# Optimization experiments

Hardware: AMD Instinct MI355X
Metric: run time of the kernel (lower is better)

Reference implementation:

```python
import jax, jax.numpy as jnp
import numpy as np
from jax.ops import segment_sum, segment_max

N = 100000   # nodes
E = 300000   # directed edges (3-regular fullerene cages)
F_IN = 16    # num_node_features
D = 128      # hidden_dim
H = 8        # heads
C = D // H   # per-head channels = 16
L = 4        # num_layers
G = 1600     # number of graphs in the batch
EPS = 1e-5   # BatchNorm eps
NEG_SLOPE = 0.2  # GATConv leaky_relu slope


def setup_inputs() -> dict:
    key = jax.random.key(0)
    ks = jax.random.split(key, 16)
    x = jax.random.normal(ks[0], (N, F_IN), jnp.float32)
    edge_index = jax.random.randint(ks[1], (2, E), 0, N, dtype=jnp.int64)
    batch = jnp.sort(jax.random.randint(ks[2], (N,), 0, G, dtype=jnp.int64))
    def w(k, shape, fan_in):
        return jax.random.normal(k, shape, jnp.float32) / np.sqrt(fan_in)
    return {
        "x": x, "edge_index": edge_index, "batch": batch,
        "Wp": w(ks[3], (F_IN, D), F_IN), "bp": jnp.zeros((D,), jnp.float32),
        "Wg": w(ks[4], (L, D, D), D),                       # per-layer GAT lin weight
        "asrc": w(ks[5], (L, H, C), C), "adst": w(ks[6], (L, H, C), C),
        "bg": jnp.zeros((L, D), jnp.float32),               # GAT bias
        "gamma": jnp.ones((L, D), jnp.float32), "beta": jnp.zeros((L, D), jnp.float32),
        "hW1": w(ks[7], (3, D, D // 2), D), "hb1": jnp.zeros((3, D // 2), jnp.float32),
        "hW2": w(ks[8], (3, D // 2, 1), D // 2), "hb2": jnp.zeros((3, 1), jnp.float32),
    }


def _gat_layer(x, W, att_src, att_dst, bias, src, dst):
    # PyG GATConv: linear transform per head, additive attention, scatter-softmax over dst
    xh = (x @ W).reshape(N, H, C)                      # [N,H,C]
    a_src = (xh * att_src).sum(-1)                     # [N,H]
    a_dst = (xh * att_dst).sum(-1)                     # [N,H]
    e = jax.nn.leaky_relu(a_src[src] + a_dst[dst], NEG_SLOPE)   # [E',H]
    m = segment_max(e, dst, num_segments=N)            # stable softmax per destination
    ex = jnp.exp(e - m[dst])
    denom = segment_sum(ex, dst, num_segments=N)       # > 0 (self-loops present)
    alpha = ex / denom[dst]                            # [E',H]
    out = segment_sum(alpha[:, :, None] * xh[src], dst, num_segments=N)  # [N,H,C]
    return out.reshape(N, D) + bias


def _forward(x, Wp, bp, Wg, asrc, adst, bg, gamma, beta, hW1, hb1, hW2, hb2,
             edge_index, batch):
    # add self loops (GATConv default add_self_loops=True)
    loop = jnp.arange(N, dtype=edge_index.dtype)
    src = jnp.concatenate([edge_index[0], loop])
    dst = jnp.concatenate([edge_index[1], loop])
    h = jax.nn.relu(x @ Wp + bp)
    for i in range(L):
        h = _gat_layer(h, Wg[i], asrc[i], adst[i], bg[i], src, dst)
        mu = h.mean(0)
        var = ((h - mu) ** 2).mean(0)                   # biased var (BN training math)
        h = (h - mu) / jnp.sqrt(var + EPS) * gamma[i] + beta[i]
        h = jax.nn.relu(h)                              # dropout off (eval)
    # global mean pool over graphs
    counts = segment_sum(jnp.ones((N,), h.dtype), batch, num_segments=G)
    pooled = segment_sum(h, batch, num_segments=G) / jnp.maximum(counts, 1.0)[:, None]
    # 3 output heads: Linear -> ReLU -> Linear(1)
    hid = jax.nn.relu(jnp.einsum('gd,kdm->kgm', pooled, hW1) + hb1[:, None, :])
    out = jnp.einsum('kgm,kmo->kgo', hid, hW2) + hb2[:, None, :]   # [3,G,1]
    return out[:, :, 0].T                               # [G,3]


def reference(x, edge_index, batch, Wp, bp, Wg, asrc, adst, bg, gamma, beta,
              hW1, hb1, hW2, hb2):
    return _forward(x, Wp, bp, Wg, asrc, adst, bg, gamma, beta,
                    hW1, hb1, hW2, hb2, edge_index, batch)
```

## Files before the change

### kernel.cpp

```cpp
#include <hip/hip_runtime.h>

#define D 128
#define NH 8
#define CH 16
#define NEG 0.2f
#define BN_EPS 1e-5f
#define MAXDEG 32
#define NSLICE 32
#define WROWS 144

typedef unsigned int uint;
typedef unsigned short ushort;
typedef __attribute__((ext_vector_type(8))) short bfrag;
typedef __attribute__((ext_vector_type(4))) float ffrag;

__device__ __forceinline__ float bf_lo(uint u){ return __uint_as_float(u << 16); }
__device__ __forceinline__ float bf_hi(uint u){ return __uint_as_float(u & 0xffff0000u); }
__device__ __forceinline__ float bf2f(ushort s){ return __uint_as_float(((uint)s) << 16); }
__device__ __forceinline__ ushort f2b(float f){
  uint u = __float_as_uint(f);
  u += 0x7fffu + ((u >> 16) & 1u);
  return (ushort)(u >> 16);
}

__global__ void k_scatter(const int* __restrict__ ei, int* __restrict__ deg,
                          int* __restrict__ col, int E){
  int e = blockIdx.x*blockDim.x + threadIdx.x;
  if (e < E){
    int d = ei[E + e];
    int pos = atomicAdd(&deg[d], 1);
    if (pos < MAXDEG) col[(size_t)d*MAXDEG + pos] = ei[e];
  }
}

__global__ void k_setup(const float* __restrict__ x, const float* __restrict__ Wp,
                        const float* __restrict__ bp, ushort* __restrict__ h,
                        const int* __restrict__ batch, int* __restrict__ gs,
                        const float* __restrict__ Wg, const float* __restrict__ asrc,
                        const float* __restrict__ adst, ushort* __restrict__ WtB,
                        int n, int G, int WTOT, int bInit, int bGb, int bWp){
  int bid = blockIdx.x;
  int t = threadIdx.x;
  if (bid < bInit){
    int i = bid*256 + t;
    if (i >= n*32) return;
    int nid = i >> 5, d4 = (i & 31)*4;
    const float* xr = x + nid*16;
    float s[4] = { bp[d4], bp[d4+1], bp[d4+2], bp[d4+3] };
#pragma unroll
    for (int k = 0; k < 16; k++){
      float xv = xr[k];
      const float* wr = Wp + k*D + d4;
      s[0] += xv*wr[0]; s[1] += xv*wr[1]; s[2] += xv*wr[2]; s[3] += xv*wr[3];
    }
    uint2 o;
    o.x = ((uint)f2b(fmaxf(s[0],0.f))) | (((uint)f2b(fmaxf(s[1],0.f))) << 16);
    o.y = ((uint)f2b(fmaxf(s[2],0.f))) | (((uint)f2b(fmaxf(s[3],0.f))) << 16);
    *(uint2*)(h + (size_t)nid*D + d4) = o;
  } else if (bid < bInit + bGb){
    int i = (bid - bInit)*256 + t;
    if (i >= n) return;
    int b = batch[i];
    int bpv = (i == 0) ? -1 : batch[i-1];
    for (int g = bpv + 1; g <= b; g++) gs[g] = i;
    if (i == n-1) for (int g = b + 1; g <= G; g++) gs[g] = n;
  } else if (bid < bInit + bGb + bWp){
    int i = (bid - bInit - bGb)*256 + t;
    if (i >= WTOT) return;
    int l = i >> 14, r = i & 16383, nn = r >> 7, kk = r & 127;
    WtB[(size_t)l*WROWS*D + nn*D + kk] = f2b(Wg[(size_t)l*16384 + kk*128 + nn]);
  } else {
    int i = (bid - bInit - bGb - bWp)*256 + t;
    int wscTot = (WTOT >> 14)*16*128;
    if (i >= wscTot) return;
    int l = i >> 11, r = i & 2047, j = r >> 7, k = r & 127;
    const float* wrow = Wg + (size_t)l*16384 + k*128;
    float s = 0.f;
    if (j < 8){
      const float* av = asrc + l*128 + j*16;
#pragma unroll
      for (int c = 0; c < 16; c++) s += wrow[j*16 + c] * av[c];
    } else {
      const float* av = adst + l*128 + (j - 8)*16;
#pragma unroll
      for (int c = 0; c < 16; c++) s += wrow[(j - 8)*16 + c] * av[c];
    }
    WtB[(size_t)l*WROWS*D + (128 + j)*D + k] = f2b(s);
  }
}

__global__ __launch_bounds__(512) void k_gemm(const ushort* __restrict__ hin,
                                              const ushort* __restrict__ WtB,
                                              ushort* __restrict__ xh,
                                              float* __restrict__ sc2,
                                              const float* __restrict__ bnsum,
                                              const float* __restrict__ gamma,
                                              const float* __restrict__ beta,
                                              int n, int first){
  __shared__ __align__(16) ushort wL[WROWS*136];
  __shared__ float sS[128], sB[128];
  int t = threadIdx.x;
  int wid = t >> 6, lane = t & 63, l15 = lane & 15, quad = lane >> 4;
  int n0 = blockIdx.x * 256;
  int rbase = wid*32;

  if (t < 128){
    float sc, sh;
    if (first){ sc = 1.f; sh = 0.f; }
    else {
      float s = 0.f, s2 = 0.f;
#pragma unroll 8
      for (int sl = 0; sl < NSLICE; sl++){
        s  += bnsum[sl*256 + t];
        s2 += bnsum[sl*256 + 128 + t];
      }
      float invn = 1.0f / (float)n;
      float mu = s * invn;
      float var = s2 * invn - mu*mu;
      sc = gamma[t] * rsqrtf(var + BN_EPS);
      sh = beta[t] - mu*sc;
    }
    sS[t] = sc; sB[t] = sh;
  }
#pragma unroll
  for (int i = 0; i < 5; i++){
    int u = t + i*512;
    if (u < WROWS*16){
      int r = u >> 4, c8 = u & 15;
      *(uint4*)(wL + r*136 + c8*8) = *(const uint4*)(WtB + (size_t)r*D + c8*8);
    }
  }
  __syncthreads();

  bfrag a[2][4];
#pragma unroll
  for (int mt = 0; mt < 2; mt++){
    int row = n0 + rbase + mt*16 + l15;
#pragma unroll
    for (int ks = 0; ks < 4; ks++){
      union { bfrag b; ushort us[8]; } in, ov;
      in.b = (bfrag){0,0,0,0,0,0,0,0};
      if (row < n) in.b = *(const bfrag*)(hin + (size_t)row*D + ks*32 + quad*8);
      int kb = ks*32 + quad*8;
#pragma unroll
      for (int j = 0; j < 8; j++){
        float f = bf2f(in.us[j])*sS[kb + j] + sB[kb + j];
        ov.us[j] = f2b(f > 0.f ? f : 0.f);
      }
      a[mt][ks] = ov.b;
    }
  }

  ffrag acc[2][9];
#pragma unroll
  for (int mt = 0; mt < 2; mt++)
#pragma unroll
    for (int nt = 0; nt < 9; nt++) acc[mt][nt] = (ffrag){0.f,0.f,0.f,0.f};

#pragma unroll
  for (int nt = 0; nt < 9; nt++){
#pragma unroll
    for (int ks = 0; ks < 4; ks++){
      bfrag b = *(const bfrag*)(wL + (nt*16 + l15)*136 + ks*32 + quad*8);
      acc[0][nt] = __builtin_amdgcn_mfma_f32_16x16x32_bf16(a[0][ks], b, acc[0][nt], 0, 0, 0);
      acc[1][nt] = __builtin_amdgcn_mfma_f32_16x16x32_bf16(a[1][ks], b, acc[1][nt], 0, 0, 0);
    }
  }

#pragma unroll
  for (int mt = 0; mt < 2; mt++)
#pragma unroll
    for (int r = 0; r < 4; r++){
      int grow = n0 + rbase + mt*16 + quad*4 + r;
      if (grow < n){
        sc2[(size_t)grow*16 + l15] = acc[mt][8][r];
        ushort* xr = xh + (size_t)grow*D + l15;
#pragma unroll
        for (int nt = 0; nt < 8; nt++)
          xr[nt*16] = f2b(acc[mt][nt][r]);
      }
    }
}

__global__ __launch_bounds__(1024) void k_agg(const uint* __restrict__ xh32,
                                              const float* __restrict__ sc2,
                                              const int* __restrict__ deg,
                                              const int* __restrict__ col,
                                              const float* __restrict__ bg,
                                              ushort* __restrict__ hout,
                                              float* __restrict__ bnsum, int n){
  int wv = threadIdx.x >> 6;
  int l  = threadIdx.x & 63;
  int hs = l & 7;
  int jc = l >> 3;
  int nid = blockIdx.x*16 + wv;

  float s0=0.f, s1=0.f, q0=0.f, q1=0.f;

  if (nid < n){
    const int* cb = col + nid*MAXDEG;
    int cnt = deg[nid];
    int idx[8];
#pragma unroll
    for (int jj = 0; jj < 8; jj++) idx[jj] = cb[jj];
    float ad = sc2[nid*16 + 8 + hs];
    float as = sc2[nid*16 + hs];
    uint selfv = xh32[nid*64 + l];
    float av = sc2[idx[jc]*16 + hs];
    float xv0[8], xv1[8];
#pragma unroll
    for (int jj = 0; jj < 8; jj++){
      uint v = xh32[idx[jj]*64 + l];
      xv0[jj] = bf_lo(v); xv1[jj] = bf_hi(v);
    }
    if (cnt > MAXDEG) cnt = MAXDEG;
    int cc = cnt < 8 ? cnt : 8;
    float e0 = as + ad; e0 = e0 > 0.f ? e0 : NEG*e0;
    float m = e0, dnm = 1.f;
    float acc0 = bf_lo(selfv), acc1 = bf_hi(selfv);

    float e = -1e30f;
    if (jc < cc){ float ee = av + ad; e = ee > 0.f ? ee : NEG*ee; }
    float mc = e;
    mc = fmaxf(mc, __shfl_xor(mc, 8));
    mc = fmaxf(mc, __shfl_xor(mc, 16));
    mc = fmaxf(mc, __shfl_xor(mc, 32));
    float mn = fmaxf(m, mc);
    float rsc = __expf(m - mn);
    float w = (jc < cc) ? __expf(e - mn) : 0.f;
    float ws = w;
    ws += __shfl_xor(ws, 8);
    ws += __shfl_xor(ws, 16);
    ws += __shfl_xor(ws, 32);
    dnm = dnm*rsc + ws;
    m = mn;
    float rc = __shfl(rsc, jc);
    acc0 *= rc; acc1 *= rc;
#pragma unroll
    for (int jj = 0; jj < 8; jj++){
      float wj = __shfl(w, jj*8 + jc);
      acc0 += wj * xv0[jj];
      acc1 += wj * xv1[jj];
    }
    for (int c0 = 8; c0 < cnt; c0 += 8){
      int cc2 = cnt - c0; if (cc2 > 8) cc2 = 8;
#pragma unroll
      for (int jj = 0; jj < 8; jj++) idx[jj] = cb[c0 + jj];
      float av2 = sc2[idx[jc]*16 + hs];
#pragma unroll
      for (int jj = 0; jj < 8; jj++){
        uint v = xh32[idx[jj]*64 + l];
        xv0[jj] = bf_lo(v); xv1[jj] = bf_hi(v);
      }
      float e2 = -1e30f;
      if (jc < cc2){ float ee = av2 + ad; e2 = ee > 0.f ? ee : NEG*ee; }
      float mc2 = e2;
      mc2 = fmaxf(mc2, __shfl_xor(mc2, 8));
      mc2 = fmaxf(mc2, __shfl_xor(mc2, 16));
      mc2 = fmaxf(mc2, __shfl_xor(mc2, 32));
      float mn2 = fmaxf(m, mc2);
      float rsc2 = __expf(m - mn2);
      float w2 = (jc < cc2) ? __expf(e2 - mn2) : 0.f;
      float ws2 = w2;
      ws2 += __shfl_xor(ws2, 8);
      ws2 += __shfl_xor(ws2, 16);
      ws2 += __shfl_xor(ws2, 32);
      dnm = dnm*rsc2 + ws2;
      m = mn2;
      float rc2 = __shfl(rsc2, jc);
      acc0 *= rc2; acc1 *= rc2;
#pragma unroll
      for (int jj = 0; jj < 8; jj++){
        float wj = __shfl(w2, jj*8 + jc);
        acc0 += wj * xv0[jj];
        acc1 += wj * xv1[jj];
      }
    }
    float df = __shfl(dnm, jc);
    float inv = 1.0f / df;
    float b0 = bg[2*l], b1 = bg[2*l + 1];
    float o0 = acc0*inv + b0, o1 = acc1*inv + b1;
    uint p = ((uint)f2b(o0)) | (((uint)f2b(o1)) << 16);
    ((uint*)hout)[nid*64 + l] = p;
    s0 = o0; s1 = o1; q0 = o0*o0; q1 = o1*o1;
  }

  __shared__ float red[16][64][4];
  red[wv][l][0] = s0; red[wv][l][1] = s1; red[wv][l][2] = q0; red[wv][l][3] = q1;
  __syncthreads();
  if (wv == 0){
    float t0 = 0.f, t1 = 0.f, t2 = 0.f, t3 = 0.f;
#pragma unroll
    for (int k = 0; k < 16; k++){
      t0 += red[k][l][0]; t1 += red[k][l][1];
      t2 += red[k][l][2]; t3 += red[k][l][3];
    }
    float* bs = bnsum + (blockIdx.x & (NSLICE - 1))*256;
    atomicAdd(&bs[2*l],       t0);
    atomicAdd(&bs[2*l + 1],   t1);
    atomicAdd(&bs[128 + 2*l], t2);
    atomicAdd(&bs[129 + 2*l], t3);
  }
}

__global__ __launch_bounds__(128) void k_poolheads(const ushort* __restrict__ h,
                                                   const int* __restrict__ gs,
                                                   const float* __restrict__ bnsum,
                                                   const float* __restrict__ gamma,
                                                   const float* __restrict__ beta,
                                                   const float* __restrict__ hW1,
                                                   const float* __restrict__ hb1,
                                                   const float* __restrict__ hW2,
                                                   const float* __restrict__ hb2,
                                                   float* __restrict__ out, int n){
  int g = blockIdx.x;
  int t = threadIdx.x;
  __shared__ float sp[128];
  int st = gs[g], en = gs[g + 1];
  float sm = 0.f, s2 = 0.f;
#pragma unroll 8
  for (int sl = 0; sl < NSLICE; sl++){
    sm += bnsum[sl*256 + t];
    s2 += bnsum[sl*256 + 128 + t];
  }
  float invn = 1.0f / (float)n;
  float mu = sm * invn;
  float var = s2 * invn - mu*mu;
  float sc = gamma[t] * rsqrtf(var + BN_EPS);
  float sh = beta[t] - mu*sc;
  float s = 0.f;
  for (int r = st; r < en; r++){
    float v = bf2f(h[(size_t)r*D + t]) * sc + sh;
    s += v > 0.f ? v : 0.f;
  }
  float cnt = (float)(en - st);
  sp[t] = s / fmaxf(cnt, 1.0f);
  __syncthreads();
  int wv = t >> 6, m = t & 63;
  for (int k = wv; k < 3; k += 2){
    float acc = hb1[k*64 + m];
    const float* w = hW1 + k*8192 + m;
#pragma unroll 16
    for (int d = 0; d < 128; d++) acc += sp[d] * w[d*64];
    float val = fmaxf(acc, 0.f) * hW2[k*64 + m];
#pragma unroll
    for (int off = 32; off; off >>= 1) val += __shfl_down(val, off);
    if (m == 0) out[(size_t)g*3 + k] = val + hb2[k];
  }
}

extern "C" void kernel_launch(void* const* d_in, const int* in_sizes, int n_in,
                              void* d_out, int out_size, void* d_ws, size_t ws_size,
                              hipStream_t stream){
  const float* x    = (const float*)d_in[0];
  const int*   ei   = (const int*)d_in[1];
  const int*   batch= (const int*)d_in[2];
  const float* Wp   = (const float*)d_in[3];
  const float* bp   = (const float*)d_in[4];
  const float* Wg   = (const float*)d_in[5];
  const float* asrc = (const float*)d_in[6];
  const float* adst = (const float*)d_in[7];
  const float* bg   = (const float*)d_in[8];
  const float* gamma= (const float*)d_in[9];
  const float* beta = (const float*)d_in[10];
  const float* hW1  = (const float*)d_in[11];
  const float* hb1  = (const float*)d_in[12];
  const float* hW2  = (const float*)d_in[13];
  const float* hb2  = (const float*)d_in[14];
  float* out = (float*)d_out;

  const int E = in_sizes[1] / 2;
  const int N = in_sizes[2];
  const int G = out_size / 3;
  const int WTOT = in_sizes[5];
  const int L = WTOT / 16384;

  char* w = (char*)d_ws;
  auto alloc = [&](size_t bytes){ char* p = w; w += (bytes + 255) & ~(size_t)255; return p; };
  ushort* h     = (ushort*)alloc((size_t)N*D*2);
  ushort* xh    = (ushort*)alloc((size_t)N*D*2);
  float* sc2    = (float*)alloc((size_t)N*16*4);
  int*   deg    = (int*)  alloc((size_t)N*4);
  int*   col    = (int*)  alloc(((size_t)N*MAXDEG + 64)*4);
  float* bnsumL = (float*)alloc((size_t)4*NSLICE*256*4);
  char*  zend   = w;
  int*   gs     = (int*)  alloc((size_t)(G + 1)*4);
  ushort* WtB   = (ushort*)alloc((size_t)L*WROWS*D*2);

  hipMemsetAsync(deg, 0, (size_t)(zend - (char*)deg), stream);
  k_scatter<<<(E + 255)/256, 256, 0, stream>>>(ei, deg, col, E);

  const int bInit = (N*32 + 255)/256;
  const int bGb   = (N + 255)/256;
  const int bWp   = (WTOT + 255)/256;
  const int bWsc  = (WTOT/8 + 255)/256;
  k_setup<<<bInit + bGb + bWp + bWsc, 256, 0, stream>>>(
      x, Wp, bp, h, batch, gs, Wg, asrc, adst, WtB,
      N, G, WTOT, bInit, bGb, bWp);

  for (int l = 0; l < 4; l++){
    float* bnPrev = bnsumL + (size_t)(l - 1)*NSLICE*256;
    float* bnCur  = bnsumL + (size_t)l*NSLICE*256;
    k_gemm<<<(N + 255)/256, 512, 0, stream>>>(h, WtB + (size_t)l*WROWS*D, xh, sc2,
                                              l == 0 ? bnCur : bnPrev,
                                              gamma + l*D, beta + l*D, N, l == 0);
    k_agg<<<(N + 15)/16, 1024, 0, stream>>>((const uint*)xh, sc2, deg, col,
                                            bg + l*D, h, bnCur, N);
  }

  k_poolheads<<<G, 128, 0, stream>>>(h, gs, bnsumL + (size_t)3*NSLICE*256,
                                     gamma + 3*D, beta + 3*D,
                                     hW1, hb1, hW2, hb2, out, N);
}
```

Baseline: 394.2 us.

## Process four nodes per wavefront in GAT aggregation to batch gathers

The aggregation kernel now has each wavefront handle four destination nodes instead of one. It loads the column indices with int4 vector loads and issues all first-chunk neighbor gathers for the four nodes together, to raise memory-level parallelism and hide gather latency. Invalid indices are clamped so the col buffer no longer needs zeroing, and it moves out of the memset range. In exchange it uses more registers per thread, launches a quarter as many waves, and creates less contention on the BN partial-sum atomics.

```diff
diff --git a/kernel.cpp b/kernel.cpp
--- a/kernel.cpp
+++ b/kernel.cpp
@@ -8,6 +8,7 @@
 #define MAXDEG 32
 #define NSLICE 32
 #define WROWS 144
+#define NPW 4
 
 typedef unsigned int uint;
 typedef unsigned short ushort;
@@ -182,116 +183,185 @@
     }
 }
 
-__global__ __launch_bounds__(1024) void k_agg(const uint* __restrict__ xh32,
-                                              const float* __restrict__ sc2,
-                                              const int* __restrict__ deg,
-                                              const int* __restrict__ col,
-                                              const float* __restrict__ bg,
-                                              ushort* __restrict__ hout,
-                                              float* __restrict__ bnsum, int n){
+__global__ __launch_bounds__(512) void k_agg(const uint* __restrict__ xh32,
+                                             const float* __restrict__ sc2,
+                                             const int* __restrict__ deg,
+                                             const int* __restrict__ col,
+                                             const float* __restrict__ bg,
+                                             ushort* __restrict__ hout,
+                                             float* __restrict__ bnsum, int n){
   int wv = threadIdx.x >> 6;
   int l  = threadIdx.x & 63;
   int hs = l & 7;
   int jc = l >> 3;
-  int nid = blockIdx.x*16 + wv;
-
-  float s0=0.f, s1=0.f, q0=0.f, q1=0.f;
-
-  if (nid < n){
-    const int* cb = col + nid*MAXDEG;
-    int cnt = deg[nid];
-    int idx[8];
-#pragma unroll
-    for (int jj = 0; jj < 8; jj++) idx[jj] = cb[jj];
-    float ad = sc2[nid*16 + 8 + hs];
-    float as = sc2[nid*16 + hs];
-    uint selfv = xh32[nid*64 + l];
-    float av = sc2[idx[jc]*16 + hs];
-    float xv0[8], xv1[8];
-#pragma unroll
-    for (int jj = 0; jj < 8; jj++){
-      uint v = xh32[idx[jj]*64 + l];
-      xv0[jj] = bf_lo(v); xv1[jj] = bf_hi(v);
-    }
-    if (cnt > MAXDEG) cnt = MAXDEG;
-    int cc = cnt < 8 ? cnt : 8;
-    float e0 = as + ad; e0 = e0 > 0.f ? e0 : NEG*e0;
-    float m = e0, dnm = 1.f;
-    float acc0 = bf_lo(selfv), acc1 = bf_hi(selfv);
-
-    float e = -1e30f;
-    if (jc < cc){ float ee = av + ad; e = ee > 0.f ? ee : NEG*ee; }
-    float mc = e;
-    mc = fmaxf(mc, __shfl_xor(mc, 8));
-    mc = fmaxf(mc, __shfl_xor(mc, 16));
-    mc = fmaxf(mc, __shfl_xor(mc, 32));
-    float mn = fmaxf(m, mc);
-    float rsc = __expf(m - mn);
-    float w = (jc < cc) ? __expf(e - mn) : 0.f;
-    float ws = w;
-    ws += __shfl_xor(ws, 8);
-    ws += __shfl_xor(ws, 16);
-    ws += __shfl_xor(ws, 32);
-    dnm = dnm*rsc + ws;
-    m = mn;
-    float rc = __shfl(rsc, jc);
-    acc0 *= rc; acc1 *= rc;
-#pragma unroll
-    for (int jj = 0; jj < 8; jj++){
-      float wj = __shfl(w, jj*8 + jc);
-      acc0 += wj * xv0[jj];
-      acc1 += wj * xv1[jj];
-    }
-    for (int c0 = 8; c0 < cnt; c0 += 8){
-      int cc2 = cnt - c0; if (cc2 > 8) cc2 = 8;
-#pragma unroll
-      for (int jj = 0; jj < 8; jj++) idx[jj] = cb[c0 + jj];
-      float av2 = sc2[idx[jc]*16 + hs];
+  int base = (blockIdx.x*8 + wv)*NPW;
+
+  float bnS0=0.f, bnS1=0.f, bnQ0=0.f, bnQ1=0.f;
+  float b0 = bg[2*l], b1 = bg[2*l + 1];
+
+  int nid[NPW], dg[NPW], myr[NPW];
+  int4 ca[NPW], cb[NPW];
+  float as_[NPW], ad_[NPW];
+  uint sf[NPW];
+#pragma unroll
+  for (int p = 0; p < NPW; p++){
+    int nn = base + p;
+    nid[p] = (nn < n) ? nn : 0;
+  }
+#pragma unroll
+  for (int p = 0; p < NPW; p++) dg[p] = deg[nid[p]];
+#pragma unroll
+  for (int p = 0; p < NPW; p++){
+    const int4* cp = (const int4*)(col + (size_t)nid[p]*MAXDEG);
+    ca[p] = cp[0]; cb[p] = cp[1];
+    myr[p] = col[(size_t)nid[p]*MAXDEG + jc];
+  }
+#pragma unroll
+  for (int p = 0; p < NPW; p++){
+    as_[p] = sc2[nid[p]*16 + hs];
+    ad_[p] = sc2[nid[p]*16 + 8 + hs];
+    sf[p]  = xh32[nid[p]*64 + l];
+  }
+
+  int id[NPW][8];
+#pragma unroll
+  for (int p = 0; p < NPW; p++){
+    id[p][0]=ca[p].x; id[p][1]=ca[p].y; id[p][2]=ca[p].z; id[p][3]=ca[p].w;
+    id[p][4]=cb[p].x; id[p][5]=cb[p].y; id[p][6]=cb[p].z; id[p][7]=cb[p].w;
+#pragma unroll
+    for (int j = 0; j < 8; j++){
+      uint u = (uint)id[p][j];
+      id[p][j] = (u < (uint)n) ? id[p][j] : nid[p];
+    }
+    uint um = (uint)myr[p];
+    myr[p] = (um < (uint)n) ? myr[p] : nid[p];
+  }
+  float av_[NPW];
+#pragma unroll
+  for (int p = 0; p < NPW; p++) av_[p] = sc2[myr[p]*16 + hs];
+  uint g[NPW][8];
+#pragma unroll
+  for (int p = 0; p < NPW; p++)
+#pragma unroll
+    for (int j = 0; j < 8; j++) g[p][j] = xh32[(size_t)id[p][j]*64 + l];
+
+  int cnt[NPW];
+#pragma unroll
+  for (int p = 0; p < NPW; p++){
+    int c = dg[p]; if (c > MAXDEG) c = MAXDEG; if (base + p >= n) c = 0;
+    cnt[p] = c;
+  }
+
+  float m_[NPW], dnm[NPW], a0[NPW], a1[NPW], e_[NPW], mc[NPW], w_[NPW], ws[NPW];
+#pragma unroll
+  for (int p = 0; p < NPW; p++){
+    float e0 = as_[p] + ad_[p]; e0 = e0 > 0.f ? e0 : NEG*e0;
+    m_[p] = e0; dnm[p] = 1.f; a0[p] = bf_lo(sf[p]); a1[p] = bf_hi(sf[p]);
+    int cc = cnt[p] < 8 ? cnt[p] : 8;
+    float ee = av_[p] + ad_[p]; ee = ee > 0.f ? ee : NEG*ee;
+    e_[p] = (jc < cc) ? ee : -1e30f;
+    mc[p] = e_[p];
+  }
+#pragma unroll
+  for (int p = 0; p < NPW; p++) mc[p] = fmaxf(mc[p], __shfl_xor(mc[p], 8));
+#pragma unroll
+  for (int p = 0; p < NPW; p++) mc[p] = fmaxf(mc[p], __shfl_xor(mc[p], 16));
+#pragma unroll
+  for (int p = 0; p < NPW; p++) mc[p] = fmaxf(mc[p], __shfl_xor(mc[p], 32));
+#pragma unroll
+  for (int p = 0; p < NPW; p++){
+    float mn = fmaxf(m_[p], mc[p]);
+    float rsc = __expf(m_[p] - mn);
+    int cc = cnt[p] < 8 ? cnt[p] : 8;
+    w_[p] = (jc < cc) ? __expf(e_[p] - mn) : 0.f;
+    ws[p] = w_[p];
+    m_[p] = mn;
+    mc[p] = rsc;
+  }
+#pragma unroll
+  for (int p = 0; p < NPW; p++) ws[p] += __shfl_xor(ws[p], 8);
+#pragma unroll
+  for (int p = 0; p < NPW; p++) ws[p] += __shfl_xor(ws[p], 16);
+#pragma unroll
+  for (int p = 0; p < NPW; p++) ws[p] += __shfl_xor(ws[p], 32);
+#pragma unroll
+  for (int p = 0; p < NPW; p++){
+    dnm[p] = dnm[p]*mc[p] + ws[p];
+    float rc = __shfl(mc[p], jc);
+    a0[p] *= rc; a1[p] *= rc;
+  }
+#pragma unroll
+  for (int jj = 0; jj < 8; jj++){
+#pragma unroll
+    for (int p = 0; p < NPW; p++){
+      float wj = __shfl(w_[p], jj*8 + jc);
+      a0[p] += wj * bf_lo(g[p][jj]);
+      a1[p] += wj * bf_hi(g[p][jj]);
+    }
+  }
+
+#pragma unroll
+  for (int p = 0; p < NPW; p++){
+    const int* cbp = col + (size_t)nid[p]*MAXDEG;
+    for (int c0 = 8; c0 < cnt[p]; c0 += 8){
+      int cc2 = cnt[p] - c0; if (cc2 > 8) cc2 = 8;
+      int id2[8];
 #pragma unroll
       for (int jj = 0; jj < 8; jj++){
-        uint v = xh32[idx[jj]*64 + l];
-        xv0[jj] = bf_lo(v); xv1[jj] = bf_hi(v);
+        int v = cbp[c0 + jj];
+        uint u = (uint)v;
+        id2[jj] = (u < (uint)n && c0 + jj < cnt[p]) ? v : nid[p];
       }
+      int my2 = cbp[c0 + jc];
+      { uint u = (uint)my2; my2 = (u < (uint)n) ? my2 : nid[p]; }
+      float av2 = sc2[my2*16 + hs];
+      uint g2[8];
+#pragma unroll
+      for (int jj = 0; jj < 8; jj++) g2[jj] = xh32[(size_t)id2[jj]*64 + l];
       float e2 = -1e30f;
-      if (jc < cc2){ float ee = av2 + ad; e2 = ee > 0.f ? ee : NEG*ee; }
+      if (jc < cc2){ float ee = av2 + ad_[p]; e2 = ee > 0.f ? ee : NEG*ee; }
       float mc2 = e2;
       mc2 = fmaxf(mc2, __shfl_xor(mc2, 8));
       mc2 = fmaxf(mc2, __shfl_xor(mc2, 16));
       mc2 = fmaxf(mc2, __shfl_xor(mc2, 32));
-      float mn2 = fmaxf(m, mc2);
-      float rsc2 = __expf(m - mn2);
+      float mn2 = fmaxf(m_[p], mc2);
+      float rsc2 = __expf(m_[p] - mn2);
       float w2 = (jc < cc2) ? __expf(e2 - mn2) : 0.f;
       float ws2 = w2;
       ws2 += __shfl_xor(ws2, 8);
       ws2 += __shfl_xor(ws2, 16);
       ws2 += __shfl_xor(ws2, 32);
-      dnm = dnm*rsc2 + ws2;
-      m = mn2;
+      dnm[p] = dnm[p]*rsc2 + ws2; m_[p] = mn2;
       float rc2 = __shfl(rsc2, jc);
-      acc0 *= rc2; acc1 *= rc2;
+      a0[p] *= rc2; a1[p] *= rc2;
 #pragma unroll
       for (int jj = 0; jj < 8; jj++){
         float wj = __shfl(w2, jj*8 + jc);
-        acc0 += wj * xv0[jj];
-        acc1 += wj * xv1[jj];
+        a0[p] += wj * bf_lo(g2[jj]);
+        a1[p] += wj * bf_hi(g2[jj]);
       }
     }
-    float df = __shfl(dnm, jc);
+  }
+
+#pragma unroll
+  for (int p = 0; p < NPW; p++){
+    float df = __shfl(dnm[p], jc);
     float inv = 1.0f / df;
-    float b0 = bg[2*l], b1 = bg[2*l + 1];
-    float o0 = acc0*inv + b0, o1 = acc1*inv + b1;
-    uint p = ((uint)f2b(o0)) | (((uint)f2b(o1)) << 16);
-    ((uint*)hout)[nid*64 + l] = p;
-    s0 = o0; s1 = o1; q0 = o0*o0; q1 = o1*o1;
-  }
-
-  __shared__ float red[16][64][4];
-  red[wv][l][0] = s0; red[wv][l][1] = s1; red[wv][l][2] = q0; red[wv][l][3] = q1;
+    float o0 = a0[p]*inv + b0, o1 = a1[p]*inv + b1;
+    if (base + p < n){
+      uint pk = ((uint)f2b(o0)) | (((uint)f2b(o1)) << 16);
+      ((uint*)hout)[(size_t)(base + p)*64 + l] = pk;
+      bnS0 += o0; bnS1 += o1; bnQ0 += o0*o0; bnQ1 += o1*o1;
+    }
+  }
+
+  __shared__ float red[8][64][4];
+  red[wv][l][0] = bnS0; red[wv][l][1] = bnS1; red[wv][l][2] = bnQ0; red[wv][l][3] = bnQ1;
   __syncthreads();
   if (wv == 0){
     float t0 = 0.f, t1 = 0.f, t2 = 0.f, t3 = 0.f;
 #pragma unroll
-    for (int k = 0; k < 16; k++){
+    for (int k = 0; k < 8; k++){
       t0 += red[k][l][0]; t1 += red[k][l][1];
       t2 += red[k][l][2]; t3 += red[k][l][3];
     }
@@ -381,9 +451,9 @@
   ushort* xh    = (ushort*)alloc((size_t)N*D*2);
   float* sc2    = (float*)alloc((size_t)N*16*4);
   int*   deg    = (int*)  alloc((size_t)N*4);
-  int*   col    = (int*)  alloc(((size_t)N*MAXDEG + 64)*4);
   float* bnsumL = (float*)alloc((size_t)4*NSLICE*256*4);
   char*  zend   = w;
+  int*   col    = (int*)  alloc(((size_t)N*MAXDEG + 64)*4);
   int*   gs     = (int*)  alloc((size_t)(G + 1)*4);
   ushort* WtB   = (ushort*)alloc((size_t)L*WROWS*D*2);
 
@@ -404,8 +474,8 @@
     k_gemm<<<(N + 255)/256, 512, 0, stream>>>(h, WtB + (size_t)l*WROWS*D, xh, sc2,
                                               l == 0 ? bnCur : bnPrev,
                                               gamma + l*D, beta + l*D, N, l == 0);
-    k_agg<<<(N + 15)/16, 1024, 0, stream>>>((const uint*)xh, sc2, deg, col,
-                                            bg + l*D, h, bnCur, N);
+    k_agg<<<(N + 8*NPW - 1)/(8*NPW), 512, 0, stream>>>((const uint*)xh, sc2, deg, col,
+                                                       bg + l*D, h, bnCur, N);
   }
 
   k_poolheads<<<G, 128, 0, stream>>>(h, gs, bnsumL + (size_t)3*NSLICE*256,
```

New measurement: 404.3 us. 1.03x slower.
